# Kernel tuning notes

Measured on AMD Instinct MI355X. Metric: run time of the kernel, lower is better.

## Reference

```python
import jax, jax.numpy as jnp
import numpy as np

D_MODEL = 128
N_HEADS = 8
N_POINTS = 8
MAX_RES = 10.0


def setup_inputs() -> dict:
    key = jax.random.key(0)
    ks = jax.random.split(key, 12)
    B, C, H, W = 4, D_MODEL, 128, 128
    nh, P = N_HEADS, N_POINTS
    inp = {
        'nbr_fea': jax.random.normal(ks[0], (B, C, H, W), jnp.float32),
        'ext_fea': jax.random.normal(ks[1], (B, C, H, W), jnp.float32),
        'flow': jax.random.normal(ks[2], (B, 2, H, W), jnp.float32) * 2.0,
        'W_off': jax.random.normal(ks[3], (C, nh * P * 2), jnp.float32) * 0.02,
        'b_off': jax.random.normal(ks[4], (nh * P * 2,), jnp.float32) * 0.02,
        'W_attn': jax.random.normal(ks[5], (C, nh * P), jnp.float32) * 0.02,
        'b_attn': jnp.zeros((nh * P,), jnp.float32),
        'W_val': jax.random.normal(ks[6], (C, C), jnp.float32) * (1.0 / np.sqrt(C)),
        'b_val': jnp.zeros((C,), jnp.float32),
        'W_out': jax.random.normal(ks[7], (C, C), jnp.float32) * (1.0 / np.sqrt(C)),
        'b_out': jnp.zeros((C,), jnp.float32),
    }
    return inp


def _bilinear_gather(value, loc, H, W):
    # value: (B, nh, HW, dh)  loc: (B, nh, Q, P, 2) normalized to [0,1]
    # grid_sample semantics: align_corners=False, zero padding
    B, nh, HW, dh = value.shape
    Q, P = loc.shape[2], loc.shape[3]
    x = loc[..., 0] * W - 0.5  # (B,nh,Q,P) pixel coords
    y = loc[..., 1] * H - 0.5
    x0 = jnp.floor(x)
    y0 = jnp.floor(y)
    wx = x - x0
    wy = y - y0
    out = jnp.zeros((B, nh, Q * P, dh), value.dtype)
    for dx, dy, wgt in ((0, 0, (1 - wx) * (1 - wy)), (1, 0, wx * (1 - wy)),
                        (0, 1, (1 - wx) * wy), (1, 1, wx * wy)):
        xi = x0 + dx
        yi = y0 + dy
        valid = (xi >= 0) & (xi < W) & (yi >= 0) & (yi < H)
        xi_c = jnp.clip(xi, 0, W - 1).astype(jnp.int32)
        yi_c = jnp.clip(yi, 0, H - 1).astype(jnp.int32)
        idx = (yi_c * W + xi_c).reshape(B, nh, Q * P, 1)
        g = jnp.take_along_axis(value, idx, axis=2)  # (B,nh,QP,dh)
        w_eff = (wgt * valid.astype(value.dtype)).reshape(B, nh, Q * P, 1)
        out = out + g * w_eff
    return out.reshape(B, nh, Q, P, dh)


def reference(nbr_fea, ext_fea, flow, W_off, b_off, W_attn, b_attn, W_val, b_val, W_out, b_out):
    B, C, H, W = nbr_fea.shape
    nh, P = N_HEADS, N_POINTS
    dh = C // nh
    Q = H * W
    # normalized reference points (pixel centers / extent)
    ys = (jnp.arange(H, dtype=jnp.float32) + 0.5) / H
    xs = (jnp.arange(W, dtype=jnp.float32) + 0.5) / W
    yy, xx = jnp.meshgrid(ys, xs, indexing='ij')
    ref = jnp.stack([xx, yy], -1).reshape(Q, 2)  # (Q,2)

    ext = ext_fea.transpose(0, 2, 3, 1).reshape(B, Q, C)
    # flow-guided sampling offsets (pixels), residue bounded by tanh
    off = MAX_RES * jnp.tanh(ext @ W_off + b_off)
    off = off.reshape(B, Q, nh, P, 2)
    flow_q = flow.transpose(0, 2, 3, 1).reshape(B, Q, 1, 1, 2)
    norm = jnp.array([W, H], jnp.float32)
    loc = ref[None, :, None, None, :] + (flow_q + off) / norm  # (B,Q,nh,P,2)

    attn = jax.nn.softmax((ext @ W_attn + b_attn).reshape(B, Q, nh, P), axis=-1)

    val = (nbr_fea.transpose(0, 2, 3, 1).reshape(B, Q, C) @ W_val + b_val)
    val = val.reshape(B, Q, nh, dh).transpose(0, 2, 1, 3)  # (B,nh,HW,dh)

    sampled = _bilinear_gather(val, loc.transpose(0, 2, 1, 3, 4), H, W)  # (B,nh,Q,P,dh)
    agg = jnp.einsum('bnqpd,bqnp->bqnd', sampled, attn).reshape(B, Q, C)
    out = agg @ W_out + b_out  # (B,Q,C)
    return out.reshape(B, H, W, C).transpose(0, 3, 1, 2)
```

## Files before the change

### kernel.cpp

```cpp
#include <hip/hip_runtime.h>
#include <math.h>

namespace {
constexpr int B   = 4;
constexpr int C   = 128;
constexpr int H   = 128;
constexpr int W   = 128;
constexpr int HWn = H * W;
constexpr int NH  = 8;
constexpr int KC  = 8;
}

using short8 = __attribute__((ext_vector_type(8))) short;
using f32x4  = __attribute__((ext_vector_type(4))) float;

__device__ __forceinline__ float fast_tanh(float x) {
  float e = __expf(2.f * x);
  return 1.f - 2.f / (e + 1.f);
}
__device__ __forceinline__ unsigned f2bf(float f) {
  unsigned u = __float_as_uint(f);
  return (u + 0x7FFFu + ((u >> 16) & 1u)) >> 16;
}
__device__ __forceinline__ unsigned pack2bf(float a, float b) {
  return f2bf(a) | (f2bf(b) << 16);
}

__global__ __launch_bounds__(256) void prep_weights_kernel(
    const float* __restrict__ Woff, const float* __restrict__ Wattn,
    const float* __restrict__ Wval,
    unsigned short* __restrict__ wcat_t, unsigned short* __restrict__ wval_t) {
  int row = blockIdx.x * 256 + threadIdx.x;
  if (row >= 320) return;
  const float* src; int ldn; int col; unsigned short* dst;
  if (row < 192) {
    if (row < 128) { src = Woff; ldn = 128; col = row; }
    else           { src = Wattn; ldn = 64; col = row - 128; }
    dst = wcat_t + row * 128;
  } else {
    src = Wval; ldn = 128; col = row - 192; dst = wval_t + (row - 192) * 128;
  }
  for (int k0 = 0; k0 < 128; k0 += 8) {
    unsigned pk[4];
#pragma unroll
    for (int j = 0; j < 4; ++j)
      pk[j] = pack2bf(src[(k0 + 2 * j) * ldn + col],
                      src[(k0 + 2 * j + 1) * ldn + col]);
    *(uint4*)(dst + k0) = make_uint4(pk[0], pk[1], pk[2], pk[3]);
  }
}

__global__ __launch_bounds__(256) void gemm_kernel(
    const float* __restrict__ nbr, const float* __restrict__ ext,
    const unsigned short* __restrict__ wval_t,
    const float* __restrict__ bv,
    const unsigned short* __restrict__ wcat_t,
    const float* __restrict__ boff, const float* __restrict__ battn,
    unsigned short* __restrict__ val, float* __restrict__ proj) {
  __shared__ unsigned short a_s[64 * 152];
  __shared__ unsigned short b_s[192 * 40];
  const int t    = threadIdx.x;
  const int grp  = blockIdx.x >> 10;
  const int id   = blockIdx.x & 1023;
  const int b    = id >> 8;
  const int q0   = (id & 255) * 64;
  const int wv   = t >> 6;
  const int lane = t & 63;
  const int li   = lane & 15, quad = lane >> 4;

  const float* Ab = (grp ? ext : nbr) + (size_t)b * C * HWn + q0;
#pragma unroll
  for (int it = 0; it < 4; ++it) {
    int idx = t + 256 * it;
    int kp  = idx >> 4;
    int q4  = (idx & 15) * 4;
    float4 fa = *(const float4*)(Ab + (size_t)(2 * kp) * HWn + q4);
    float4 fb = *(const float4*)(Ab + (size_t)(2 * kp + 1) * HWn + q4);
    const float* pa = &fa.x; const float* pb = &fb.x;
#pragma unroll
    for (int j = 0; j < 4; ++j)
      *(unsigned*)&a_s[(q4 + j) * 152 + 2 * kp] = pack2bf(pa[j], pb[j]);
  }

  if (grp == 0) {
    f32x4 acc[8];
#pragma unroll
    for (int n = 0; n < 8; ++n) acc[n] = (f32x4){0.f, 0.f, 0.f, 0.f};

    for (int ck = 0; ck < 4; ++ck) {
      __syncthreads();
#pragma unroll
      for (int it = 0; it < 2; ++it) {
        int idx = t + 256 * it;
        int n = idx >> 2, seg = idx & 3;
        *(uint4*)&b_s[n * 40 + seg * 8] =
            *(const uint4*)(wval_t + n * 128 + ck * 32 + seg * 8);
      }
      __syncthreads();
      short8 af = *(const short8*)&a_s[(16 * wv + li) * 152 + ck * 32 + quad * 8];
#pragma unroll
      for (int n = 0; n < 8; ++n) {
        short8 bfr = *(const short8*)&b_s[(16 * n + li) * 40 + quad * 8];
        acc[n] = __builtin_amdgcn_mfma_f32_16x16x32_bf16(af, bfr, acc[n], 0, 0, 0);
      }
    }

    __syncthreads();
#pragma unroll
    for (int n = 0; n < 8; ++n) {
      float bias = bv[16 * n + li];
#pragma unroll
      for (int reg = 0; reg < 4; ++reg) {
        int q = 16 * wv + 4 * quad + reg;
        a_s[q * 152 + 16 * n + li] = (unsigned short)f2bf(acc[n][reg] + bias);
      }
    }
    __syncthreads();
    {
      const int qi = t & 63, r = t >> 6;
      uint4 v0 = *(const uint4*)&a_s[qi * 152 + 32 * r];
      uint4 v1 = *(const uint4*)&a_s[qi * 152 + 32 * r + 8];
      uint4 v2 = *(const uint4*)&a_s[qi * 152 + 32 * r + 16];
      uint4 v3 = *(const uint4*)&a_s[qi * 152 + 32 * r + 24];
      unsigned short* d0 = val + ((size_t)(b * NH + 2 * r) * HWn + q0 + qi) * 16;
      unsigned short* d1 = val + ((size_t)(b * NH + 2 * r + 1) * HWn + q0 + qi) * 16;
      *(uint4*)d0 = v0; *(uint4*)(d0 + 8) = v1;
      *(uint4*)d1 = v2; *(uint4*)(d1 + 8) = v3;
    }
  } else {
    f32x4 acc[12];
#pragma unroll
    for (int n = 0; n < 12; ++n) acc[n] = (f32x4){0.f, 0.f, 0.f, 0.f};

    for (int ck = 0; ck < 4; ++ck) {
      __syncthreads();
#pragma unroll
      for (int it = 0; it < 3; ++it) {
        int idx = t + 256 * it;
        int n = idx >> 2, seg = idx & 3;
        *(uint4*)&b_s[n * 40 + seg * 8] =
            *(const uint4*)(wcat_t + n * 128 + ck * 32 + seg * 8);
      }
      __syncthreads();
      short8 af = *(const short8*)&a_s[(16 * wv + li) * 152 + ck * 32 + quad * 8];
#pragma unroll
      for (int n = 0; n < 12; ++n) {
        short8 bfr = *(const short8*)&b_s[(16 * n + li) * 40 + quad * 8];
        acc[n] = __builtin_amdgcn_mfma_f32_16x16x32_bf16(af, bfr, acc[n], 0, 0, 0);
      }
    }

#pragma unroll
    for (int n = 0; n < 12; ++n) {
      int col = 16 * n + li;
      float bias = (col < 128) ? boff[col] : battn[col - 128];
#pragma unroll
      for (int reg = 0; reg < 4; ++reg) {
        int q = 16 * wv + 4 * quad + reg;
        proj[(size_t)(b * HWn + q0 + q) * 192 + col] = acc[n][reg] + bias;
      }
    }
  }
}

__global__ __launch_bounds__(256) void gather_out_kernel(
    const float* __restrict__ flow, const float* __restrict__ proj,
    const unsigned short* __restrict__ val,
    const float* __restrict__ Wout, const float* __restrict__ bout,
    float* __restrict__ out) {
  __shared__ float agg_s[C * 32];
  __shared__ float w_s[KC * 128];
  const int t  = threadIdx.x;
  const int qi = t & 31;
  const int r  = t >> 5;

  const int blk  = blockIdx.x;
  const int lin  = (blk & 7) * 256 + (blk >> 3);
  const int b    = lin >> 9;
  const int tile = lin & 511;
  const int x0   = (tile & 7) * 16;
  const int y0   = (tile >> 3) * 2;
  const int x    = x0 + (qi & 15);
  const int y    = y0 + (qi >> 4);

  const float* pp = proj + (size_t)(b * HWn + y * W + x) * 192;
  float offa[16];
  float atta[8];
#pragma unroll
  for (int j4 = 0; j4 < 4; ++j4) {
    float4 v = *(const float4*)(pp + 16 * r + 4 * j4);
    offa[4 * j4 + 0] = 10.f * fast_tanh(v.x);
    offa[4 * j4 + 1] = 10.f * fast_tanh(v.y);
    offa[4 * j4 + 2] = 10.f * fast_tanh(v.z);
    offa[4 * j4 + 3] = 10.f * fast_tanh(v.w);
  }
#pragma unroll
  for (int j4 = 0; j4 < 2; ++j4) {
    float4 v = *(const float4*)(pp + 128 + 8 * r + 4 * j4);
    atta[4 * j4 + 0] = v.x; atta[4 * j4 + 1] = v.y;
    atta[4 * j4 + 2] = v.z; atta[4 * j4 + 3] = v.w;
  }
  {
    float m = atta[0];
#pragma unroll
    for (int p = 1; p < 8; ++p) m = fmaxf(m, atta[p]);
    float s = 0.f;
#pragma unroll
    for (int p = 0; p < 8; ++p) { float ev = __expf(atta[p] - m); atta[p] = ev; s += ev; }
    float inv = 1.f / s;
#pragma unroll
    for (int p = 0; p < 8; ++p) atta[p] *= inv;
  }

  const float xb = (float)x + flow[(size_t)b * 2 * HWn + y * W + x];
  const float yb = (float)y + flow[((size_t)b * 2 + 1) * HWn + y * W + x];

  float agg[16];
#pragma unroll
  for (int j = 0; j < 16; ++j) agg[j] = 0.f;
  const unsigned short* valh =
      val + ((size_t)b * NH + r) * HWn * 16;

#pragma unroll
  for (int p = 0; p < 8; ++p) {
    float sx = xb + offa[2 * p];
    float sy = yb + offa[2 * p + 1];
    float x0f = floorf(sx), y0f = floorf(sy);
    float wx = sx - x0f, wy = sy - y0f;
    int ix0 = (int)x0f, iy0 = (int)y0f;
    int ix1 = ix0 + 1,  iy1 = iy0 + 1;
    float aw  = atta[p];
    float w00 = aw * (1.f - wx) * (1.f - wy);
    float w10 = aw * wx * (1.f - wy);
    float w01 = aw * (1.f - wx) * wy;
    float w11 = aw * wx * wy;
    if ((unsigned)ix0 >= (unsigned)W) { w00 = 0.f; w01 = 0.f; }
    if ((unsigned)ix1 >= (unsigned)W) { w10 = 0.f; w11 = 0.f; }
    if ((unsigned)iy0 >= (unsigned)H) { w00 = 0.f; w10 = 0.f; }
    if ((unsigned)iy1 >= (unsigned)H) { w01 = 0.f; w11 = 0.f; }
    int x0c = min(max(ix0, 0), W - 1);
    int x1c = min(max(ix1, 0), W - 1);
    int y0c = min(max(iy0, 0), H - 1);
    int y1c = min(max(iy1, 0), H - 1);
    const unsigned short* c00 = valh + (size_t)(y0c * W + x0c) * 16;
    const unsigned short* c10 = valh + (size_t)(y0c * W + x1c) * 16;
    const unsigned short* c01 = valh + (size_t)(y1c * W + x0c) * 16;
    const unsigned short* c11 = valh + (size_t)(y1c * W + x1c) * 16;
#pragma unroll
    for (int cn = 0; cn < 4; ++cn) {
      const unsigned short* cp = (cn == 0) ? c00 : (cn == 1) ? c10
                                : (cn == 2) ? c01 : c11;
      float wgt = (cn == 0) ? w00 : (cn == 1) ? w10 : (cn == 2) ? w01 : w11;
      uint4 ga = ((const uint4*)cp)[0];
      uint4 gb = ((const uint4*)cp)[1];
      unsigned gs[8] = {ga.x, ga.y, ga.z, ga.w, gb.x, gb.y, gb.z, gb.w};
#pragma unroll
      for (int i = 0; i < 8; ++i) {
        float lo = __uint_as_float(gs[i] << 16);
        float hi = __uint_as_float(gs[i] & 0xFFFF0000u);
        agg[2 * i]     += wgt * lo;
        agg[2 * i + 1] += wgt * hi;
      }
    }
  }

#pragma unroll
  for (int j = 0; j < 16; ++j) agg_s[(16 * r + j) * 32 + qi] = agg[j];

  float acc[16];
#pragma unroll
  for (int j = 0; j < 16; ++j) acc[j] = bout[16 * r + j];

  for (int ck = 0; ck < C / KC; ++ck) {
    const int k0 = ck * KC;
    {
      int k = t >> 5, col = (t & 31) * 4;
      *(float4*)&w_s[k * 128 + col] =
          *(const float4*)(Wout + (size_t)(k0 + k) * 128 + col);
    }
    __syncthreads();
#pragma unroll
    for (int k = 0; k < KC; ++k) {
      float a = agg_s[(k0 + k) * 32 + qi];
      const float4* wp = (const float4*)&w_s[k * 128 + 16 * r];
#pragma unroll
      for (int j4 = 0; j4 < 4; ++j4) {
        float4 w = wp[j4];
        acc[4 * j4 + 0] += a * w.x; acc[4 * j4 + 1] += a * w.y;
        acc[4 * j4 + 2] += a * w.z; acc[4 * j4 + 3] += a * w.w;
      }
    }
    __syncthreads();
  }

  float* ob = out + (size_t)b * C * HWn + y * W + x;
#pragma unroll
  for (int j = 0; j < 16; ++j)
    ob[(size_t)(16 * r + j) * HWn] = acc[j];
}

extern "C" void kernel_launch(void* const* d_in, const int* in_sizes, int n_in,
                              void* d_out, int out_size, void* d_ws, size_t ws_size,
                              hipStream_t stream) {
  const float* nbr   = (const float*)d_in[0];
  const float* extf  = (const float*)d_in[1];
  const float* flow  = (const float*)d_in[2];
  const float* Woff  = (const float*)d_in[3];
  const float* boff  = (const float*)d_in[4];
  const float* Wattn = (const float*)d_in[5];
  const float* battn = (const float*)d_in[6];
  const float* Wval  = (const float*)d_in[7];
  const float* bval  = (const float*)d_in[8];
  const float* Wout  = (const float*)d_in[9];
  const float* bout  = (const float*)d_in[10];
  float* outp = (float*)d_out;

  unsigned short* val    = (unsigned short*)d_ws;
  unsigned short* wcat_t = val + (size_t)B * NH * HWn * 16;
  unsigned short* wval_t = wcat_t + 192 * 128;
  float*          proj   = (float*)(wval_t + 128 * 128);

  prep_weights_kernel<<<dim3(2), dim3(256), 0, stream>>>(
      Woff, Wattn, Wval, wcat_t, wval_t);
  gemm_kernel<<<dim3(2048), dim3(256), 0, stream>>>(
      nbr, extf, wval_t, bval, wcat_t, boff, battn, val, proj);
  gather_out_kernel<<<dim3(2048), dim3(256), 0, stream>>>(
      flow, proj, val, Wout, bout, outp);
}
```

Before: 235.1 us.

## Use bf16 MFMA for output projection in gather kernel

Replaces the scalar FP32 output projection in the gather kernel with bf16 MFMA 16x16x32 instructions. Wout is pre-transposed to bf16 in the prep kernel, and the aggregated features go into shared memory as bf16. Results are staged through padded shared memory so global stores stay coalesced. The shared footprint shrinks and launch bounds are raised to allow more resident blocks, at the cost of lower precision in the final projection.

```diff
diff --git a/kernel.cpp b/kernel.cpp
--- a/kernel.cpp
+++ b/kernel.cpp
@@ -8,7 +8,6 @@
 constexpr int W   = 128;
 constexpr int HWn = H * W;
 constexpr int NH  = 8;
-constexpr int KC  = 8;
 }
 
 using short8 = __attribute__((ext_vector_type(8))) short;
@@ -28,17 +27,20 @@
 
 __global__ __launch_bounds__(256) void prep_weights_kernel(
     const float* __restrict__ Woff, const float* __restrict__ Wattn,
-    const float* __restrict__ Wval,
-    unsigned short* __restrict__ wcat_t, unsigned short* __restrict__ wval_t) {
+    const float* __restrict__ Wval, const float* __restrict__ Wout,
+    unsigned short* __restrict__ wcat_t, unsigned short* __restrict__ wval_t,
+    unsigned short* __restrict__ wout_t) {
   int row = blockIdx.x * 256 + threadIdx.x;
-  if (row >= 320) return;
+  if (row >= 448) return;
   const float* src; int ldn; int col; unsigned short* dst;
   if (row < 192) {
     if (row < 128) { src = Woff; ldn = 128; col = row; }
     else           { src = Wattn; ldn = 64; col = row - 128; }
     dst = wcat_t + row * 128;
+  } else if (row < 320) {
+    src = Wval; ldn = 128; col = row - 192; dst = wval_t + (row - 192) * 128;
   } else {
-    src = Wval; ldn = 128; col = row - 192; dst = wval_t + (row - 192) * 128;
+    src = Wout; ldn = 128; col = row - 320; dst = wout_t + (row - 320) * 128;
   }
   for (int k0 = 0; k0 < 128; k0 += 8) {
     unsigned pk[4];
@@ -163,13 +165,15 @@
   }
 }
 
-__global__ __launch_bounds__(256) void gather_out_kernel(
+__global__ __launch_bounds__(256, 8) void gather_out_kernel(
     const float* __restrict__ flow, const float* __restrict__ proj,
     const unsigned short* __restrict__ val,
-    const float* __restrict__ Wout, const float* __restrict__ bout,
+    const unsigned short* __restrict__ wout_t, const float* __restrict__ bout,
     float* __restrict__ out) {
-  __shared__ float agg_s[C * 32];
-  __shared__ float w_s[KC * 128];
+  __shared__ float smem[128 * 33];
+  unsigned short* a_s2 = (unsigned short*)smem;
+  float* c_s = smem;
+
   const int t  = threadIdx.x;
   const int qi = t & 31;
   const int r  = t >> 5;
@@ -264,39 +268,54 @@
     }
   }
 
-#pragma unroll
-  for (int j = 0; j < 16; ++j) agg_s[(16 * r + j) * 32 + qi] = agg[j];
-
-  float acc[16];
-#pragma unroll
-  for (int j = 0; j < 16; ++j) acc[j] = bout[16 * r + j];
-
-  for (int ck = 0; ck < C / KC; ++ck) {
-    const int k0 = ck * KC;
-    {
-      int k = t >> 5, col = (t & 31) * 4;
-      *(float4*)&w_s[k * 128 + col] =
-          *(const float4*)(Wout + (size_t)(k0 + k) * 128 + col);
-    }
-    __syncthreads();
-#pragma unroll
-    for (int k = 0; k < KC; ++k) {
-      float a = agg_s[(k0 + k) * 32 + qi];
-      const float4* wp = (const float4*)&w_s[k * 128 + 16 * r];
-#pragma unroll
-      for (int j4 = 0; j4 < 4; ++j4) {
-        float4 w = wp[j4];
-        acc[4 * j4 + 0] += a * w.x; acc[4 * j4 + 1] += a * w.y;
-        acc[4 * j4 + 2] += a * w.z; acc[4 * j4 + 3] += a * w.w;
-      }
-    }
-    __syncthreads();
-  }
+  {
+    unsigned pk[8];
+#pragma unroll
+    for (int j = 0; j < 8; ++j) pk[j] = pack2bf(agg[2 * j], agg[2 * j + 1]);
+    uint4* dst = (uint4*)&a_s2[qi * 136 + 16 * r];
+    dst[0] = make_uint4(pk[0], pk[1], pk[2], pk[3]);
+    dst[1] = make_uint4(pk[4], pk[5], pk[6], pk[7]);
+  }
+  __syncthreads();
+
+  const int lane = t & 63;
+  const int li   = lane & 15, quad = lane >> 4;
+  const int wv   = t >> 6;
+  const int mt   = wv & 1;
+  const int ng   = (wv >> 1) * 4;
+
+  f32x4 acc[4];
+#pragma unroll
+  for (int i = 0; i < 4; ++i) acc[i] = (f32x4){0.f, 0.f, 0.f, 0.f};
+
+#pragma unroll
+  for (int ks = 0; ks < 4; ++ks) {
+    short8 af = *(const short8*)&a_s2[(mt * 16 + li) * 136 + ks * 32 + quad * 8];
+#pragma unroll
+    for (int i = 0; i < 4; ++i) {
+      short8 bfr = *(const short8*)(wout_t + (size_t)(16 * (ng + i) + li) * 128 +
+                                    ks * 32 + quad * 8);
+      acc[i] = __builtin_amdgcn_mfma_f32_16x16x32_bf16(af, bfr, acc[i], 0, 0, 0);
+    }
+  }
+  __syncthreads();
+
+#pragma unroll
+  for (int i = 0; i < 4; ++i) {
+    int c = 16 * (ng + i) + li;
+    float bias = bout[c];
+#pragma unroll
+    for (int reg = 0; reg < 4; ++reg) {
+      int q = mt * 16 + quad * 4 + reg;
+      c_s[c * 33 + q] = acc[i][reg] + bias;
+    }
+  }
+  __syncthreads();
 
   float* ob = out + (size_t)b * C * HWn + y * W + x;
 #pragma unroll
   for (int j = 0; j < 16; ++j)
-    ob[(size_t)(16 * r + j) * HWn] = acc[j];
+    ob[(size_t)(16 * r + j) * HWn] = c_s[(16 * r + j) * 33 + qi];
 }
 
 extern "C" void kernel_launch(void* const* d_in, const int* in_sizes, int n_in,
@@ -318,12 +337,13 @@
   unsigned short* val    = (unsigned short*)d_ws;
   unsigned short* wcat_t = val + (size_t)B * NH * HWn * 16;
   unsigned short* wval_t = wcat_t + 192 * 128;
-  float*          proj   = (float*)(wval_t + 128 * 128);
+  unsigned short* wout_t = wval_t + 128 * 128;
+  float*          proj   = (float*)(wout_t + 128 * 128);
 
   prep_weights_kernel<<<dim3(2), dim3(256), 0, stream>>>(
-      Woff, Wattn, Wval, wcat_t, wval_t);
+      Woff, Wattn, Wval, Wout, wcat_t, wval_t, wout_t);
   gemm_kernel<<<dim3(2048), dim3(256), 0, stream>>>(
       nbr, extf, wval_t, bval, wcat_t, boff, battn, val, proj);
   gather_out_kernel<<<dim3(2048), dim3(256), 0, stream>>>(
-      flow, proj, val, Wout, bout, outp);
-}
+      flow, proj, val, wout_t, bout, outp);
+}
```

After: 798.9 us. 3.4x slower.
